# Kernel optimization log

Hardware: AMD Instinct MI355X
Metric: run time of the kernel (lower is better)

## Reference

```python
import jax, jax.numpy as jnp
import numpy as np

N = 50000    # nodes
E = 800000   # edges (avg degree 16)
B = 256      # graphs in the batch (static for segment ops)
H = 128      # feature / hidden width (channels[-2])
NL = 4       # LSTM layers in Set2Set
PS = 4       # Set2Set processing steps
OUT = 2      # channels[-1]


def _bn(h, g, b):
    # BatchNorm1d with batch statistics (training-mode math, biased variance)
    m = h.mean(0)
    v = jnp.mean((h - m) ** 2, 0)
    return (h - m) * jax.lax.rsqrt(v + 1e-5) * g + b


def _gin(x, src, dst, W1, b1, ga1, be1, W2, b2, ga2, be2):
    # GINConv, eps=0: out = MLP(x + sum_{j->i} x_j)
    agg = jax.ops.segment_sum(x[src], dst, num_segments=x.shape[0])
    h = x + agg
    h = jax.nn.relu(_bn(h @ W1.T + b1, ga1, be1))
    h = jax.nn.relu(_bn(h @ W2.T + b2, ga2, be2))
    return h


def _set2set(x, batch, Wih0, Whh0, b0, WihR, WhhR, bR):
    hs = [jnp.zeros((B, H), x.dtype)] * NL
    cs = [jnp.zeros((B, H), x.dtype)] * NL
    q_star = jnp.zeros((B, 2 * H), x.dtype)
    for _ in range(PS):
        inp = q_star
        nhs, ncs = [], []
        for l in range(NL):  # stacked LSTM cells, seq-len 1 per step
            Wih = Wih0 if l == 0 else WihR[l - 1]
            Whh = Whh0 if l == 0 else WhhR[l - 1]
            bb = b0 if l == 0 else bR[l - 1]
            gates = inp @ Wih.T + hs[l] @ Whh.T + bb
            i, f, g, o = jnp.split(gates, 4, axis=-1)  # torch gate order i,f,g,o
            c = jax.nn.sigmoid(f) * cs[l] + jax.nn.sigmoid(i) * jnp.tanh(g)
            h = jax.nn.sigmoid(o) * jnp.tanh(c)
            nhs.append(h); ncs.append(c)
            inp = h
        hs, cs = nhs, ncs
        q = inp  # (B, H) top-layer hidden
        # per-graph segment softmax attention
        e = jnp.sum(x * q[batch], -1)                        # (N,)
        m = jax.ops.segment_max(e, batch, num_segments=B)
        ee = jnp.exp(e - m[batch])
        s = jax.ops.segment_sum(ee, batch, num_segments=B)
        a = ee / s[batch]
        r = jax.ops.segment_sum(a[:, None] * x, batch, num_segments=B)  # (B, H)
        q_star = jnp.concatenate([q, r], -1)
    return q_star


def setup_inputs() -> dict:
    key = jax.random.key(0)
    ks = jax.random.split(key, 16)

    def w(k, shape):
        return jax.random.normal(k, shape, jnp.float32) * 0.05

    d = {}
    d["x"] = jax.random.normal(ks[0], (N, H), jnp.float32)
    d["edge_index"] = jax.random.randint(ks[1], (2, E), 0, N, dtype=jnp.int32)
    d["batch"] = jnp.sort(jax.random.randint(ks[2], (N,), 0, B, dtype=jnp.int32))
    for i, g in enumerate(("g0", "g1")):
        kk = jax.random.split(ks[3 + i], 2)
        d[g + "_W1"] = w(kk[0], (H, H)); d[g + "_b1"] = jnp.zeros((H,), jnp.float32)
        d[g + "_gamma1"] = jnp.ones((H,), jnp.float32); d[g + "_beta1"] = jnp.zeros((H,), jnp.float32)
        d[g + "_W2"] = w(kk[1], (H, H)); d[g + "_b2"] = jnp.zeros((H,), jnp.float32)
        d[g + "_gamma2"] = jnp.ones((H,), jnp.float32); d[g + "_beta2"] = jnp.zeros((H,), jnp.float32)
    d["Wih0"] = w(ks[6], (4 * H, 2 * H))
    d["Whh0"] = w(ks[7], (4 * H, H))
    d["b0"] = jnp.zeros((4 * H,), jnp.float32)
    d["WihR"] = w(ks[8], (NL - 1, 4 * H, H))
    d["WhhR"] = w(ks[9], (NL - 1, 4 * H, H))
    d["bR"] = jnp.zeros((NL - 1, 4 * H), jnp.float32)
    d["lin_W"] = w(ks[10], (OUT, 2 * H))
    d["lin_b"] = jnp.zeros((OUT,), jnp.float32)
    return d


def reference(x, edge_index, batch,
              g0_W1, g0_b1, g0_gamma1, g0_beta1, g0_W2, g0_b2, g0_gamma2, g0_beta2,
              g1_W1, g1_b1, g1_gamma1, g1_beta1, g1_W2, g1_b2, g1_gamma2, g1_beta2,
              Wih0, Whh0, b0, WihR, WhhR, bR, lin_W, lin_b):
    src, dst = edge_index[0], edge_index[1]
    x = _gin(x, src, dst, g0_W1, g0_b1, g0_gamma1, g0_beta1, g0_W2, g0_b2, g0_gamma2, g0_beta2)
    x = _gin(x, src, dst, g1_W1, g1_b1, g1_gamma1, g1_beta1, g1_W2, g1_b2, g1_gamma2, g1_beta2)
    q = _set2set(x, batch, Wih0, Whh0, b0, WihR, WhhR, bR)
    # F.dropout(p=0.1) is identity in eval mode
    return q @ lin_W.T + lin_b
```

## Files before the change

kernel.cpp:

```cpp
#include <hip/hip_runtime.h>
#include <math.h>

#define NN 50000
#define EE 800000
#define BBG 256
#define HHC 128
#define SEG_CAP 448
#define ESC 512
#define NBIN 196
#define NBLK 196

typedef _Float16 half8 __attribute__((ext_vector_type(8)));
typedef _Float16 half4 __attribute__((ext_vector_type(4)));
typedef _Float16 half2v __attribute__((ext_vector_type(2)));

#if defined(__has_builtin)
#if __has_builtin(__builtin_amdgcn_fdot2)
#define USE_FDOT2 1
#endif
#endif

__device__ __forceinline__ float fdot2f(half2v a, half2v b, float c) {
#ifdef USE_FDOT2
  return __builtin_amdgcn_fdot2(a, b, c, false);
#else
  return fmaf((float)a[0], (float)b[0], fmaf((float)a[1], (float)b[1], c));
#endif
}

__device__ __forceinline__ float fsigm(float x) {
  return __builtin_amdgcn_rcpf(1.f + __expf(-x));
}
__device__ __forceinline__ float ftanh(float x) {
  return 1.f - 2.f * __builtin_amdgcn_rcpf(1.f + __expf(2.f * x));
}

__device__ __forceinline__ float4 aff4(float4 v, float4 sc, float4 sh) {
  v.x = fmaxf(fmaf(v.x, sc.x, sh.x), 0.f);
  v.y = fmaxf(fmaf(v.y, sc.y, sh.y), 0.f);
  v.z = fmaxf(fmaf(v.z, sc.z, sh.z), 0.f);
  v.w = fmaxf(fmaf(v.w, sc.w, sh.w), 0.f);
  return v;
}
__device__ __forceinline__ void add4(float4& a, float4 b) {
  a.x += b.x; a.y += b.y; a.z += b.z; a.w += b.w;
}
__device__ __forceinline__ float4 cvt4(half4 h) {
  return make_float4((float)h[0], (float)h[1], (float)h[2], (float)h[3]);
}

__global__ __launch_bounds__(256) void prep_all_kernel(
    const int* __restrict__ batch,
    const int* __restrict__ ei,
    const float* __restrict__ W0, const float* __restrict__ W1,
    const float* __restrict__ W2, const float* __restrict__ W3,
    const float* __restrict__ Wih0, const float* __restrict__ Whh0,
    const float* __restrict__ WihR, const float* __restrict__ WhhR,
    const float* __restrict__ b0, const float* __restrict__ bR,
    const float* __restrict__ xsrc,
    float* __restrict__ stats, int* __restrict__ gptr, int* __restrict__ partial,
    float* __restrict__ ginWT, _Float16* __restrict__ WT0h,
    _Float16* __restrict__ WTRh, float* __restrict__ bc0, float* __restrict__ bcR,
    _Float16* __restrict__ x16a) {
  __shared__ int hist[NBIN];
  int blk = blockIdx.x, tid = threadIdx.x;
  if (blk == 0) {
    ((float4*)stats)[tid] = make_float4(0.f, 0.f, 0.f, 0.f);
    return;
  }
  if (blk <= 196) {
    int i = (blk - 1) * 256 + tid;
    if (i >= NN) return;
    int b = batch[i];
    int prev = (i == 0) ? -1 : batch[i - 1];
    for (int g = prev + 1; g <= b; ++g) gptr[g] = i;
    if (i == NN - 1) {
      for (int g = b + 1; g <= BBG; ++g) gptr[g] = NN;
    }
    return;
  }
  if (blk <= 392) {
    int b = blk - 197;
    if (tid < NBIN) hist[tid] = 0;
    __syncthreads();
    const int4* dst4 = (const int4*)(ei + EE);
#pragma unroll
    for (int c = 0; c < 4; ++c) {
      int idx = b * 1024 + c * 256 + tid;
      if (idx < EE / 4) {
        int4 d = dst4[idx];
        atomicAdd(&hist[d.x >> 8], 1);
        atomicAdd(&hist[d.y >> 8], 1);
        atomicAdd(&hist[d.z >> 8], 1);
        atomicAdd(&hist[d.w >> 8], 1);
      }
    }
    __syncthreads();
    if (tid < NBIN) partial[tid * NBLK + b] = hist[tid];
    return;
  }
  if (blk >= 2961) {
    int i = (blk - 2961) * 256 + tid;
    float4 v = ((const float4*)xsrc)[i];
    half4 h;
    h[0] = (_Float16)v.x; h[1] = (_Float16)v.y;
    h[2] = (_Float16)v.z; h[3] = (_Float16)v.w;
    ((half4*)x16a)[i] = h;
    return;
  }
  int idx = (blk - 393) * 256 + tid;
  if (idx < 65536) {
    int m = idx >> 14;
    int r = idx & 16383;
    int k = r >> 7, o = r & 127;
    const float* W = (m == 0) ? W0 : (m == 1) ? W1 : (m == 2) ? W2 : W3;
    ginWT[idx] = W[o * 128 + k];
  } else if (idx < 262144) {
    int t = idx - 65536;
    int k = t >> 9, op = t & 511;
    int j = op >> 2, g = op & 3;
    int row = g * 128 + j;
    float v = (k < 256) ? Wih0[row * 256 + k] : Whh0[row * 128 + (k - 256)];
    WT0h[((k >> 1) << 10) | (op << 1) | (k & 1)] = (_Float16)v;
  } else if (idx < 655360) {
    int t = idx - 262144;
    int l = t >> 17;
    int rem = t & 131071;
    int k = rem >> 9, op = rem & 511;
    int j = op >> 2, g = op & 3;
    int row = g * 128 + j;
    float v = (k < 128) ? WihR[((size_t)l * 512 + row) * 128 + k]
                        : WhhR[((size_t)l * 512 + row) * 128 + (k - 128)];
    WTRh[((size_t)l << 17) | ((k >> 1) << 10) | (op << 1) | (k & 1)] = (_Float16)v;
  } else {
    int t = idx - 655360;
    if (t < 512) {
      bc0[t] = b0[(t & 3) * 128 + (t >> 2)];
    } else {
      int u = t - 512;
      int l = u >> 9, op = u & 511;
      bcR[u] = bR[l * 512 + (op & 3) * 128 + (op >> 2)];
    }
  }
}


__global__ void scan_partials_kernel(const int* __restrict__ partial,
                                     int* __restrict__ block_base, int* __restrict__ total) {
  __shared__ int buf[256];
  int bin = blockIdx.x, tid = threadIdx.x;
  int v = (tid < NBLK) ? partial[bin * NBLK + tid] : 0;
  buf[tid] = v;
  __syncthreads();
  for (int off = 1; off < 256; off <<= 1) {
    int t = (tid >= off) ? buf[tid - off] : 0;
    __syncthreads();
    buf[tid] += t;
    __syncthreads();
  }
  if (tid < NBLK) block_base[bin * NBLK + tid] = buf[tid] - v;
  if (tid == 255) total[bin] = buf[255];
}

__global__ void scan_totals_kernel(const int* __restrict__ total, int* __restrict__ coarse_base) {
  __shared__ int buf[256];
  int tid = threadIdx.x;
  int v = (tid < NBIN) ? total[tid] : 0;
  buf[tid] = v;
  __syncthreads();
  for (int off = 1; off < 256; off <<= 1) {
    int t = (tid >= off) ? buf[tid - off] : 0;
    __syncthreads();
    buf[tid] += t;
    __syncthreads();
  }
  if (tid < NBIN) coarse_base[tid] = buf[tid] - v;
  if (tid == 255) coarse_base[NBIN] = buf[255];
}

__global__ __launch_bounds__(256) void bucket_scatter_kernel(const int* __restrict__ ei,
                                                             const int* __restrict__ coarse_base,
                                                             const int* __restrict__ block_base,
                                                             int* __restrict__ packed) {
  __shared__ int cursor[NBIN];
  int tid = threadIdx.x, b = blockIdx.x;
  if (tid < NBIN) cursor[tid] = coarse_base[tid] + block_base[tid * NBLK + b];
  __syncthreads();
  const int4* src4 = (const int4*)ei;
  const int4* dst4 = (const int4*)(ei + EE);
#pragma unroll
  for (int c = 0; c < 4; ++c) {
    int idx = b * 1024 + c * 256 + tid;
    if (idx < EE / 4) {
      int4 s = src4[idx];
      int4 d = dst4[idx];
      int p;
      p = atomicAdd(&cursor[d.x >> 8], 1); packed[p] = (s.x << 8) | (d.x & 255);
      p = atomicAdd(&cursor[d.y >> 8], 1); packed[p] = (s.y << 8) | (d.y & 255);
      p = atomicAdd(&cursor[d.z >> 8], 1); packed[p] = (s.z << 8) | (d.z & 255);
      p = atomicAdd(&cursor[d.w >> 8], 1); packed[p] = (s.w << 8) | (d.w & 255);
    }
  }
}

__global__ __launch_bounds__(256) void csr_finalize_kernel(const int* __restrict__ packed,
                                                           const int* __restrict__ coarse_base,
                                                           int* __restrict__ row_start,
                                                           int* __restrict__ csr) {
  __shared__ int fh[256];
  __shared__ int fb[256];
  int bin = blockIdx.x, tid = threadIdx.x;
  int e0 = coarse_base[bin], e1 = coarse_base[bin + 1];
  fh[tid] = 0;
  __syncthreads();
  for (int e = e0 + tid; e < e1; e += 256) atomicAdd(&fh[packed[e] & 255], 1);
  __syncthreads();
  int v = fh[tid];
  fb[tid] = v;
  __syncthreads();
  for (int off = 1; off < 256; off <<= 1) {
    int t = (tid >= off) ? fb[tid - off] : 0;
    __syncthreads();
    fb[tid] += t;
    __syncthreads();
  }
  int excl = fb[tid] - v;
  int node = bin * 256 + tid;
  if (node < NN) row_start[node] = e0 + excl;
  if (bin == NBIN - 1 && tid == 0) row_start[NN] = EE;
  __syncthreads();
  fb[tid] = excl;
  __syncthreads();
  for (int e = e0 + tid; e < e1; e += 256) {
    int p = packed[e];
    int pos = atomicAdd(&fb[p & 255], 1);
    csr[e0 + pos] = p >> 8;
  }
}


template <bool AFF>
__global__ __launch_bounds__(256) void gin_agg_kernel(
    const _Float16* __restrict__ x16, const int* __restrict__ row_start,
    const int* __restrict__ csr,
    const float* __restrict__ stats, const float* __restrict__ gamma,
    const float* __restrict__ beta, float* __restrict__ outp) {
  __shared__ float sc_s[128], sh_s[128];
  if (AFF) {
    int t = threadIdx.x;
    if (t < 128) {
      const float invN = 1.0f / (float)NN;
      float mm = stats[t] * invN;
      float vv = stats[128 + t] * invN - mm * mm;
      float rs = rsqrtf(vv + 1e-5f);
      float sc = gamma[t] * rs;
      sc_s[t] = sc;
      sh_s[t] = beta[t] - mm * sc;
    }
    __syncthreads();
  }
  int node = blockIdx.x * 4 + (threadIdx.x >> 6);
  int lane = threadIdx.x & 63;
  int half = lane >> 5, ln = lane & 31;
  const half4* xh = (const half4*)x16;
  float4 sc4 = make_float4(0.f, 0.f, 0.f, 0.f), sh4 = sc4;
  if (AFF) {
    sc4 = *(const float4*)&sc_s[4 * ln];
    sh4 = *(const float4*)&sh_s[4 * ln];
  }
  int s0 = row_start[node], s1 = row_start[node + 1];
  float4 self = cvt4(xh[(size_t)node * 32 + ln]);
  if (AFF) self = aff4(self, sc4, sh4);
  float4 c0 = make_float4(0.f, 0.f, 0.f, 0.f), c1 = c0, c2 = c0, c3 = c0;
  int cnt = s1 - s0;
  int mainEnd = s0 + (cnt & ~15);
  for (int j = s0; j < mainEnd; j += 16) {
    int i0 = csr[j + half + 0];
    int i1 = csr[j + half + 2];
    int i2 = csr[j + half + 4];
    int i3 = csr[j + half + 6];
    int i4 = csr[j + half + 8];
    int i5 = csr[j + half + 10];
    int i6 = csr[j + half + 12];
    int i7 = csr[j + half + 14];
    half4 h0 = xh[(size_t)i0 * 32 + ln];
    half4 h1 = xh[(size_t)i1 * 32 + ln];
    half4 h2 = xh[(size_t)i2 * 32 + ln];
    half4 h3 = xh[(size_t)i3 * 32 + ln];
    half4 h4 = xh[(size_t)i4 * 32 + ln];
    half4 h5 = xh[(size_t)i5 * 32 + ln];
    half4 h6 = xh[(size_t)i6 * 32 + ln];
    half4 h7 = xh[(size_t)i7 * 32 + ln];
    float4 v0 = cvt4(h0);
    float4 v1 = cvt4(h1);
    float4 v2 = cvt4(h2);
    float4 v3 = cvt4(h3);
    float4 v4 = cvt4(h4);
    float4 v5 = cvt4(h5);
    float4 v6 = cvt4(h6);
    float4 v7 = cvt4(h7);
    if (AFF) {
      v0 = aff4(v0, sc4, sh4); v1 = aff4(v1, sc4, sh4);
      v2 = aff4(v2, sc4, sh4); v3 = aff4(v3, sc4, sh4);
      v4 = aff4(v4, sc4, sh4); v5 = aff4(v5, sc4, sh4);
      v6 = aff4(v6, sc4, sh4); v7 = aff4(v7, sc4, sh4);
    }
    add4(c0, v0); add4(c1, v1); add4(c2, v2); add4(c3, v3);
    add4(c0, v4); add4(c1, v5); add4(c2, v6); add4(c3, v7);
  }
  for (int j = mainEnd + half; j < s1; j += 2) {
    int i = csr[j];
    float4 v = cvt4(xh[(size_t)i * 32 + ln]);
    if (AFF) v = aff4(v, sc4, sh4);
    add4(c0, v);
  }
  float4 t;
  t.x = (c0.x + c1.x) + (c2.x + c3.x);
  t.y = (c0.y + c1.y) + (c2.y + c3.y);
  t.z = (c0.z + c1.z) + (c2.z + c3.z);
  t.w = (c0.w + c1.w) + (c2.w + c3.w);
  t.x += __shfl_xor(t.x, 32);
  t.y += __shfl_xor(t.y, 32);
  t.z += __shfl_xor(t.z, 32);
  t.w += __shfl_xor(t.w, 32);
  t.x += self.x; t.y += self.y; t.z += self.z; t.w += self.w;
  if (half == 0) ((float4*)outp)[(size_t)node * 32 + ln] = t;
}

template <bool BN>
__global__ __launch_bounds__(256) void gemm_gin_kernel(
    const float* __restrict__ A, const float* __restrict__ WT,
    const float* __restrict__ bias,
    const float* __restrict__ stats, const float* __restrict__ gamma,
    const float* __restrict__ beta,
    float* __restrict__ C, _Float16* __restrict__ h16out,
    float* __restrict__ ssum, float* __restrict__ ssq, int M) {
  __shared__ float As[64][132];
  __shared__ float Wt[128][68];
  __shared__ float bsc[128], bsh[128];
  int tid = threadIdx.x;
  if (BN) {
    if (tid < 128) {
      const float invN = 1.0f / (float)NN;
      float mm = stats[tid] * invN;
      float vv = stats[128 + tid] * invN - mm * mm;
      float rs = rsqrtf(vv + 1e-5f);
      float sc = gamma[tid] * rs;
      bsc[tid] = sc;
      bsh[tid] = beta[tid] - mm * sc;
    }
    __syncthreads();
  }
  int tx = tid & 15, ty = tid >> 4;
  int bx = blockIdx.x & 1, by = blockIdx.x >> 1;
  int row0 = by * 64, c0 = bx * 64;
#pragma unroll
  for (int i = 0; i < 8; ++i) {
    int slot = tid + i * 256;
    int r = slot >> 5, k4 = (slot & 31) << 2;
    float4 v = make_float4(0.f, 0.f, 0.f, 0.f);
    if (row0 + r < M) v = *(const float4*)(A + (size_t)(row0 + r) * 128 + k4);
    if (BN) {
      v.x = fmaxf(fmaf(v.x, bsc[k4 + 0], bsh[k4 + 0]), 0.f);
      v.y = fmaxf(fmaf(v.y, bsc[k4 + 1], bsh[k4 + 1]), 0.f);
      v.z = fmaxf(fmaf(v.z, bsc[k4 + 2], bsh[k4 + 2]), 0.f);
      v.w = fmaxf(fmaf(v.w, bsc[k4 + 3], bsh[k4 + 3]), 0.f);
    }
    *(float4*)&As[r][k4] = v;
  }
#pragma unroll
  for (int i = 0; i < 8; ++i) {
    int slot = tid + i * 256;
    int k = slot >> 4, c4 = (slot & 15) << 2;
    *(float4*)&Wt[k][c4] = *(const float4*)(WT + (size_t)k * 128 + c0 + c4);
  }
  __syncthreads();
  float acc[4][4];
#pragma unroll
  for (int i = 0; i < 4; ++i)
#pragma unroll
    for (int j = 0; j < 4; ++j) acc[i][j] = 0.f;
#pragma unroll 4
  for (int kk = 0; kk < 128; kk += 4) {
    float4 w0 = *(const float4*)&Wt[kk + 0][tx << 2];
    float4 w1 = *(const float4*)&Wt[kk + 1][tx << 2];
    float4 w2 = *(const float4*)&Wt[kk + 2][tx << 2];
    float4 w3 = *(const float4*)&Wt[kk + 3][tx << 2];
#pragma unroll
    for (int i = 0; i < 4; ++i) {
      float4 a = *(const float4*)&As[(ty << 2) + i][kk];
      acc[i][0] += a.x * w0.x + a.y * w1.x + a.z * w2.x + a.w * w3.x;
      acc[i][1] += a.x * w0.y + a.y * w1.y + a.z * w2.y + a.w * w3.y;
      acc[i][2] += a.x * w0.z + a.y * w1.z + a.z * w2.z + a.w * w3.z;
      acc[i][3] += a.x * w0.w + a.y * w1.w + a.z * w2.w + a.w * w3.w;
    }
  }
  __syncthreads();
  float b0v = bias[c0 + (tx << 2) + 0];
  float b1v = bias[c0 + (tx << 2) + 1];
  float b2v = bias[c0 + (tx << 2) + 2];
  float b3v = bias[c0 + (tx << 2) + 3];
  float psum[4] = {0.f, 0.f, 0.f, 0.f}, psq[4] = {0.f, 0.f, 0.f, 0.f};
#pragma unroll
  for (int i = 0; i < 4; ++i) {
    int r = row0 + (ty << 2) + i;
    if (r < M) {
      float4 v;
      v.x = acc[i][0] + b0v; v.y = acc[i][1] + b1v;
      v.z = acc[i][2] + b2v; v.w = acc[i][3] + b3v;
      if (C) *(float4*)(C + (size_t)r * 128 + c0 + (tx << 2)) = v;
      if (h16out) {
        half4 hv;
        hv[0] = (_Float16)v.x; hv[1] = (_Float16)v.y;
        hv[2] = (_Float16)v.z; hv[3] = (_Float16)v.w;
        *(half4*)(h16out + (size_t)r * 128 + c0 + (tx << 2)) = hv;
      }
      psum[0] += v.x; psum[1] += v.y; psum[2] += v.z; psum[3] += v.w;
      psq[0] += v.x * v.x; psq[1] += v.y * v.y; psq[2] += v.z * v.z; psq[3] += v.w * v.w;
    }
  }
  float* red = &As[0][0];
#pragma unroll
  for (int j = 0; j < 4; ++j) {
    red[ty * 68 + (tx << 2) + j] = psum[j];
    red[1088 + ty * 68 + (tx << 2) + j] = psq[j];
  }
  __syncthreads();
  if (tid < 64) {
    float s = 0.f, sq = 0.f;
#pragma unroll
    for (int t = 0; t < 16; ++t) { s += red[t * 68 + tid]; sq += red[1088 + t * 68 + tid]; }
    atomicAdd(&ssum[c0 + tid], s);
    atomicAdd(&ssq[c0 + tid], sq);
  }
}

__global__ void __launch_bounds__(1024) set2set_kernel(
    const float* __restrict__ x, const int* __restrict__ gptr,
    const float* __restrict__ stats, const float* __restrict__ gamma,
    const float* __restrict__ beta,
    const _Float16* __restrict__ WT0h, const _Float16* __restrict__ WTRh,
    const float* __restrict__ bc0, const float* __restrict__ bcR,
    float* __restrict__ ebuf,
    const float* __restrict__ linW, const float* __restrict__ linb,
    float* __restrict__ out) {
  __shared__ half2v xs[SEG_CAP * 64];
  __shared__ float wpart[16][512];
  __shared__ float gates[512];
  __shared__ half2v inp2[192];
  __shared__ float hcs[4][128];
  __shared__ float ccs[4][128];
  __shared__ float qst[256];
  __shared__ float es[ESC];
  __shared__ float bsc[128], bsh[128];
  __shared__ float wred[16];
  __shared__ float smax_s, ssum_s;
  __shared__ float fred[2][4];

  int g = blockIdx.x, tid = threadIdx.x;
  int w16 = tid >> 6, lane = tid & 63;

  if (tid < 128) {
    const float invN = 1.0f / (float)NN;
    float mm = stats[tid] * invN;
    float vv = stats[128 + tid] * invN - mm * mm;
    float rs = rsqrtf(vv + 1e-5f);
    float sc = gamma[tid] * rs;
    bsc[tid] = sc;
    bsh[tid] = beta[tid] - mm * sc;
#pragma unroll
    for (int l = 0; l < 4; ++l) { hcs[l][tid] = 0.f; ccs[l][tid] = 0.f; }
  }
  if (tid < 256) qst[tid] = 0.f;
  __syncthreads();

  int s0 = gptr[g], s1 = gptr[g + 1];
  int seg = s1 - s0;
  int ncache = seg < SEG_CAP ? seg : SEG_CAP;
  const float2* x2 = (const float2*)x;
  float sc0 = bsc[2 * lane], sc1 = bsc[2 * lane + 1];
  float sh0 = bsh[2 * lane], sh1 = bsh[2 * lane + 1];
  for (int n = w16; n < ncache; n += 16) {
    float2 v = x2[(size_t)(s0 + n) * 64 + lane];
    half2v h;
    h[0] = (_Float16)fmaxf(fmaf(v.x, sc0, sh0), 0.f);
    h[1] = (_Float16)fmaxf(fmaf(v.y, sc1, sh1), 0.f);
    xs[n * 64 + lane] = h;
  }
  __syncthreads();

  int s_ = tid >> 6, cg = tid & 63;

  for (int step = 0; step < 4; ++step) {
    for (int cell = 0; cell < 4; ++cell) {
      const _Float16* WTh; const float* bias; int KP2;
      if (cell == 0) {
        WTh = WT0h; bias = bc0; KP2 = 12;
        if (tid < 192) {
          int k = tid << 1;
          float va, vb;
          if (k < 256) { va = qst[k]; vb = qst[k + 1]; }
          else { va = hcs[0][k - 256]; vb = hcs[0][k - 255]; }
          half2v h; h[0] = (_Float16)va; h[1] = (_Float16)vb;
          inp2[tid] = h;
        }
      } else {
        WTh = WTRh + (size_t)(cell - 1) * 131072;
        bias = bcR + (cell - 1) * 512; KP2 = 8;
        if (tid < 128) {
          int k = tid << 1;
          float va, vb;
          if (k < 128) { va = hcs[cell - 1][k]; vb = hcs[cell - 1][k + 1]; }
          else { va = hcs[cell][k - 128]; vb = hcs[cell][k - 127]; }
          half2v h; h[0] = (_Float16)va; h[1] = (_Float16)vb;
          inp2[tid] = h;
        }
      }
      __syncthreads();
      if (step == 0 && cell == 0) {
        if (tid < 512) gates[tid] = bias[tid];
        __syncthreads();
      } else {
        int se = (s_ + g) & 15;
        int k20 = se * KP2;
        float a0 = 0.f, a1 = 0.f, a2 = 0.f, a3 = 0.f;
        float a4 = 0.f, a5 = 0.f, a6 = 0.f, a7 = 0.f;
        if (step != 0 || se < 8) {
          const char* wb = (const char*)WTh + (size_t)k20 * 2048 + (cg << 5);
#pragma unroll 4
          for (int k2 = 0; k2 < KP2; ++k2) {
            uint4 wa = *(const uint4*)(wb + (size_t)k2 * 2048);
            uint4 wc = *(const uint4*)(wb + (size_t)k2 * 2048 + 16);
            half2v i2 = inp2[k20 + k2];
            a0 = fdot2f(i2, __builtin_bit_cast(half2v, wa.x), a0);
            a1 = fdot2f(i2, __builtin_bit_cast(half2v, wa.y), a1);
            a2 = fdot2f(i2, __builtin_bit_cast(half2v, wa.z), a2);
            a3 = fdot2f(i2, __builtin_bit_cast(half2v, wa.w), a3);
            a4 = fdot2f(i2, __builtin_bit_cast(half2v, wc.x), a4);
            a5 = fdot2f(i2, __builtin_bit_cast(half2v, wc.y), a5);
            a6 = fdot2f(i2, __builtin_bit_cast(half2v, wc.z), a6);
            a7 = fdot2f(i2, __builtin_bit_cast(half2v, wc.w), a7);
          }
        }
        *(float4*)&wpart[s_][cg << 3] = make_float4(a0, a1, a2, a3);
        *(float4*)(&wpart[s_][cg << 3] + 4) = make_float4(a4, a5, a6, a7);
        __syncthreads();
        if (tid < 512) {
          float acc = bias[tid];
#pragma unroll
          for (int s = 0; s < 16; ++s) acc += wpart[s][tid];
          gates[tid] = acc;
        }
        __syncthreads();
      }
      if (tid < 128) {
        int j = tid;
        float gi = gates[4 * j + 0];
        float gf = gates[4 * j + 1];
        float gc = gates[4 * j + 2];
        float go = gates[4 * j + 3];
        float cp = ccs[cell][j];
        float si = fsigm(gi);
        float sf = fsigm(gf);
        float so = fsigm(go);
        float cn = sf * cp + si * ftanh(gc);
        ccs[cell][j] = cn;
        hcs[cell][j] = so * ftanh(cn);
      }
      __syncthreads();
    }
    float* rpart = &wpart[0][0];
    float qx = hcs[3][2 * lane], qy = hcs[3][2 * lane + 1];
    half2v q2; q2[0] = (_Float16)qx; q2[1] = (_Float16)qy;
    float wmax = -3.0e38f;
    for (int n = w16; n < seg; n += 16) {
      float e;
      if (n < ncache) {
        e = fdot2f(xs[n * 64 + lane], q2, 0.f);
      } else {
        float2 v = x2[(size_t)(s0 + n) * 64 + lane];
        float vx = fmaxf(fmaf(v.x, sc0, sh0), 0.f);
        float vy = fmaxf(fmaf(v.y, sc1, sh1), 0.f);
        e = vx * qx + vy * qy;
      }
#pragma unroll
      for (int sh = 32; sh; sh >>= 1) e += __shfl_xor(e, sh);
      if (lane == 0) { if (n < ESC) es[n] = e; else ebuf[s0 + n] = e; }
      wmax = fmaxf(wmax, e);
    }
    if (lane == 0) wred[w16] = wmax;
    __syncthreads();
    if (tid == 0) {
      float m = wred[0];
#pragma unroll
      for (int t = 1; t < 16; ++t) m = fmaxf(m, wred[t]);
      smax_s = m;
    }
    __syncthreads();
    float m = smax_s;
    float loc = 0.f;
    for (int n = tid; n < seg; n += 1024) {
      float e = (n < ESC) ? es[n] : ebuf[s0 + n];
      float ex = __expf(e - m);
      if (n < ESC) es[n] = ex; else ebuf[s0 + n] = ex;
      loc += ex;
    }
#pragma unroll
    for (int sh = 32; sh; sh >>= 1) loc += __shfl_xor(loc, sh);
    __syncthreads();
    if (lane == 0) wred[w16] = loc;
    __syncthreads();
    if (tid == 0) {
      float s = 0.f;
#pragma unroll
      for (int t = 0; t < 16; ++t) s += wred[t];
      ssum_s = s;
    }
    __syncthreads();
    float inv = 1.0f / ssum_s;
    float rx = 0.f, ry = 0.f;
    for (int n = w16; n < seg; n += 16) {
      float ex = (n < ESC) ? es[n] : ebuf[s0 + n];
      float coef = ex * inv;
      float vx, vy;
      if (n < ncache) {
        half2v v2 = xs[n * 64 + lane];
        vx = (float)v2[0]; vy = (float)v2[1];
      } else {
        float2 v = x2[(size_t)(s0 + n) * 64 + lane];
        vx = fmaxf(fmaf(v.x, sc0, sh0), 0.f);
        vy = fmaxf(fmaf(v.y, sc1, sh1), 0.f);
      }
      rx += coef * vx; ry += coef * vy;
    }
    rpart[w16 * 128 + 2 * lane] = rx;
    rpart[w16 * 128 + 2 * lane + 1] = ry;
    __syncthreads();
    if (tid < 128) {
      float r = 0.f;
#pragma unroll
      for (int t = 0; t < 16; ++t) r += rpart[t * 128 + tid];
      qst[tid] = hcs[3][tid];
      qst[128 + tid] = r;
    }
    __syncthreads();
  }
  if (tid < 256) {
    float val = qst[tid];
    float p0 = val * linW[tid];
    float p1 = val * linW[256 + tid];
#pragma unroll
    for (int sh = 32; sh; sh >>= 1) { p0 += __shfl_xor(p0, sh); p1 += __shfl_xor(p1, sh); }
    if (lane == 0) { fred[0][w16] = p0; fred[1][w16] = p1; }
  }
  __syncthreads();
  if (tid == 0) {
    out[2 * g + 0] = fred[0][0] + fred[0][1] + fred[0][2] + fred[0][3] + linb[0];
    out[2 * g + 1] = fred[1][0] + fred[1][1] + fred[1][2] + fred[1][3] + linb[1];
  }
}


extern "C" void kernel_launch(void* const* d_in, const int* in_sizes, int n_in,
                              void* d_out, int out_size, void* d_ws, size_t ws_size,
                              hipStream_t stream) {
  const float* x = (const float*)d_in[0];
  const int* ei = (const int*)d_in[1];
  const int* batch = (const int*)d_in[2];
  const float* gW[4]  = {(const float*)d_in[3],  (const float*)d_in[7],
                         (const float*)d_in[11], (const float*)d_in[15]};
  const float* gb[4]  = {(const float*)d_in[4],  (const float*)d_in[8],
                         (const float*)d_in[12], (const float*)d_in[16]};
  const float* gga[4] = {(const float*)d_in[5],  (const float*)d_in[9],
                         (const float*)d_in[13], (const float*)d_in[17]};
  const float* gbe[4] = {(const float*)d_in[6],  (const float*)d_in[10],
                         (const float*)d_in[14], (const float*)d_in[18]};
  const float* Wih0 = (const float*)d_in[19];
  const float* Whh0 = (const float*)d_in[20];
  const float* b0   = (const float*)d_in[21];
  const float* WihR = (const float*)d_in[22];
  const float* WhhR = (const float*)d_in[23];
  const float* bR   = (const float*)d_in[24];
  const float* linW = (const float*)d_in[25];
  const float* linb = (const float*)d_in[26];
  float* out = (float*)d_out;

  char* base = (char*)d_ws;
  size_t off = 0;
  auto allocf = [&](size_t n) { float* p = (float*)(base + off); off += n * sizeof(float); return p; };
  float* xa    = allocf(6400000);
  float* xb    = allocf(6400000);
  float* ginWT = allocf(65536);
  _Float16* WT0h = (_Float16*)(base + off); off += 196608 * 2;
  _Float16* WTRh = (_Float16*)(base + off); off += 393216 * 2;
  _Float16* x16a = (_Float16*)(base + off); off += 6400000 * 2;
  _Float16* x16b = (_Float16*)(base + off); off += 6400000 * 2;
  float* bc0   = allocf(512);
  float* bcR   = allocf(1536);
  float* ebuf  = allocf(50000);
  float* stats = allocf(1024);
  int* row_start = (int*)(base + off); off += 50004 * 4;
  int* gptr = (int*)(base + off); off += 260 * 4;
  int* csr = (int*)(base + off); off += 800000 * 4;
  int* packed = (int*)(base + off); off += 800000 * 4;
  int* partial = (int*)(base + off); off += NBIN * NBLK * 4;
  int* block_base = (int*)(base + off); off += NBIN * NBLK * 4;
  int* total = (int*)(base + off); off += 256 * 4;
  int* coarse_base = (int*)(base + off); off += 260 * 4;
  (void)ws_size; (void)in_sizes; (void)n_in; (void)out_size;

  prep_all_kernel<<<9211, 256, 0, stream>>>(batch, ei, gW[0], gW[1], gW[2], gW[3],
                                            Wih0, Whh0, WihR, WhhR, b0, bR, x,
                                            stats, gptr, partial, ginWT, WT0h, WTRh,
                                            bc0, bcR, x16a);
  scan_partials_kernel<<<NBIN, 256, 0, stream>>>(partial, block_base, total);
  scan_totals_kernel<<<1, 256, 0, stream>>>(total, coarse_base);
  bucket_scatter_kernel<<<NBLK, 256, 0, stream>>>(ei, coarse_base, block_base, packed);
  csr_finalize_kernel<<<NBIN, 256, 0, stream>>>(packed, coarse_base, row_start, csr);

  gin_agg_kernel<false><<<12500, 256, 0, stream>>>(x16a, row_start, csr,
                                                   nullptr, nullptr, nullptr, xb);
  gemm_gin_kernel<false><<<1564, 256, 0, stream>>>(xb, ginWT + 0 * 16384, gb[0],
                                                   nullptr, nullptr, nullptr,
                                                   xa, nullptr, stats + 0, stats + 128, NN);
  gemm_gin_kernel<true><<<1564, 256, 0, stream>>>(xa, ginWT + 1 * 16384, gb[1],
                                                  stats + 0, gga[0], gbe[0],
                                                  nullptr, x16b, stats + 256, stats + 384, NN);
  gin_agg_kernel<true><<<12500, 256, 0, stream>>>(x16b, row_start, csr,
                                                  stats + 256, gga[1], gbe[1], xa);
  gemm_gin_kernel<false><<<1564, 256, 0, stream>>>(xa, ginWT + 2 * 16384, gb[2],
                                                   nullptr, nullptr, nullptr,
                                                   xb, nullptr, stats + 512, stats + 640, NN);
  gemm_gin_kernel<true><<<1564, 256, 0, stream>>>(xb, ginWT + 3 * 16384, gb[3],
                                                  stats + 512, gga[2], gbe[2],
                                                  xa, nullptr, stats + 768, stats + 896, NN);

  set2set_kernel<<<256, 1024, 0, stream>>>(xa, gptr, stats + 768, gga[3], gbe[3],
                                           WT0h, WTRh, bc0, bcR, ebuf, linW, linb, out);
}
```

Measured before the change: 495.6 us.

## Replace FP32 SIMT GIN GEMMs with fp16 MFMA kernels and fp16 intermediates

The four GIN linear layers now run on MFMA 16x16x32 f16 instructions. Weights are stored untransposed in fp16 and held in registers, and each block handles four 16-row tiles. The intermediate activation between the two linears of each GIN layer is written as fp16 (x16a) instead of fp32, which reduces memory traffic. BN statistics are reduced with wave shuffles. This trades accuracy, since inputs are rounded to fp16, and the output stores are strided scalar writes rather than vectorized ones.

```diff
diff --git a/kernel.cpp b/kernel.cpp
--- a/kernel.cpp
+++ b/kernel.cpp
@@ -13,6 +13,7 @@
 typedef _Float16 half8 __attribute__((ext_vector_type(8)));
 typedef _Float16 half4 __attribute__((ext_vector_type(4)));
 typedef _Float16 half2v __attribute__((ext_vector_type(2)));
+typedef float f32x4 __attribute__((ext_vector_type(4)));
 
 #if defined(__has_builtin)
 #if __has_builtin(__builtin_amdgcn_fdot2)
@@ -59,7 +60,7 @@
     const float* __restrict__ b0, const float* __restrict__ bR,
     const float* __restrict__ xsrc,
     float* __restrict__ stats, int* __restrict__ gptr, int* __restrict__ partial,
-    float* __restrict__ ginWT, _Float16* __restrict__ WT0h,
+    _Float16* __restrict__ ginWh, _Float16* __restrict__ WT0h,
     _Float16* __restrict__ WTRh, float* __restrict__ bc0, float* __restrict__ bcR,
     _Float16* __restrict__ x16a) {
   __shared__ int hist[NBIN];
@@ -112,9 +113,8 @@
   if (idx < 65536) {
     int m = idx >> 14;
     int r = idx & 16383;
-    int k = r >> 7, o = r & 127;
     const float* W = (m == 0) ? W0 : (m == 1) ? W1 : (m == 2) ? W2 : W3;
-    ginWT[idx] = W[o * 128 + k];
+    ginWh[idx] = (_Float16)W[r];
   } else if (idx < 262144) {
     int t = idx - 65536;
     int k = t >> 9, op = t & 511;
@@ -327,17 +327,16 @@
   if (half == 0) ((float4*)outp)[(size_t)node * 32 + ln] = t;
 }
 
-template <bool BN>
-__global__ __launch_bounds__(256) void gemm_gin_kernel(
-    const float* __restrict__ A, const float* __restrict__ WT,
+template <bool BN, bool AH>
+__global__ __launch_bounds__(256) void gemm_gin_mfma_kernel(
+    const float* __restrict__ A, const _Float16* __restrict__ A16,
+    const _Float16* __restrict__ Wh,
     const float* __restrict__ bias,
     const float* __restrict__ stats, const float* __restrict__ gamma,
     const float* __restrict__ beta,
     float* __restrict__ C, _Float16* __restrict__ h16out,
-    float* __restrict__ ssum, float* __restrict__ ssq, int M) {
-  __shared__ float As[64][132];
-  __shared__ float Wt[128][68];
-  __shared__ float bsc[128], bsh[128];
+    float* __restrict__ ssum, float* __restrict__ ssq) {
+  __shared__ float bsc_s[128], bsh_s[128];
   int tid = threadIdx.x;
   if (BN) {
     if (tid < 128) {
@@ -346,92 +345,104 @@
       float vv = stats[128 + tid] * invN - mm * mm;
       float rs = rsqrtf(vv + 1e-5f);
       float sc = gamma[tid] * rs;
-      bsc[tid] = sc;
-      bsh[tid] = beta[tid] - mm * sc;
-    }
-    __syncthreads();
-  }
-  int tx = tid & 15, ty = tid >> 4;
-  int bx = blockIdx.x & 1, by = blockIdx.x >> 1;
-  int row0 = by * 64, c0 = bx * 64;
-#pragma unroll
-  for (int i = 0; i < 8; ++i) {
-    int slot = tid + i * 256;
-    int r = slot >> 5, k4 = (slot & 31) << 2;
-    float4 v = make_float4(0.f, 0.f, 0.f, 0.f);
-    if (row0 + r < M) v = *(const float4*)(A + (size_t)(row0 + r) * 128 + k4);
-    if (BN) {
-      v.x = fmaxf(fmaf(v.x, bsc[k4 + 0], bsh[k4 + 0]), 0.f);
-      v.y = fmaxf(fmaf(v.y, bsc[k4 + 1], bsh[k4 + 1]), 0.f);
-      v.z = fmaxf(fmaf(v.z, bsc[k4 + 2], bsh[k4 + 2]), 0.f);
-      v.w = fmaxf(fmaf(v.w, bsc[k4 + 3], bsh[k4 + 3]), 0.f);
-    }
-    *(float4*)&As[r][k4] = v;
-  }
-#pragma unroll
-  for (int i = 0; i < 8; ++i) {
-    int slot = tid + i * 256;
-    int k = slot >> 4, c4 = (slot & 15) << 2;
-    *(float4*)&Wt[k][c4] = *(const float4*)(WT + (size_t)k * 128 + c0 + c4);
-  }
-  __syncthreads();
-  float acc[4][4];
-#pragma unroll
-  for (int i = 0; i < 4; ++i)
-#pragma unroll
-    for (int j = 0; j < 4; ++j) acc[i][j] = 0.f;
-#pragma unroll 4
-  for (int kk = 0; kk < 128; kk += 4) {
-    float4 w0 = *(const float4*)&Wt[kk + 0][tx << 2];
-    float4 w1 = *(const float4*)&Wt[kk + 1][tx << 2];
-    float4 w2 = *(const float4*)&Wt[kk + 2][tx << 2];
-    float4 w3 = *(const float4*)&Wt[kk + 3][tx << 2];
+      bsc_s[tid] = sc;
+      bsh_s[tid] = beta[tid] - mm * sc;
+    }
+    __syncthreads();
+  }
+  int w = tid >> 6, l = tid & 63;
+  int lr = l & 15, lg = l >> 4;
+  int cb = w * 32;
+  half8 bf0[4], bf1[4];
+#pragma unroll
+  for (int ks = 0; ks < 4; ++ks) {
+    int k = ks * 32 + lg * 8;
+    bf0[ks] = *(const half8*)(Wh + (size_t)(cb + lr) * 128 + k);
+    bf1[ks] = *(const half8*)(Wh + (size_t)(cb + 16 + lr) * 128 + k);
+  }
+  float bv0 = bias[cb + lr], bv1 = bias[cb + 16 + lr];
+  float ps0 = 0.f, pq0 = 0.f, ps1 = 0.f, pq1 = 0.f;
+  int t0 = blockIdx.x * 4;
+  for (int t = 0; t < 4; ++t) {
+    int tile = t0 + t;
+    if (tile >= 3125) break;
+    int r = tile * 16 + lr;
+    half8 af[4];
+#pragma unroll
+    for (int ks = 0; ks < 4; ++ks) {
+      int k0 = ks * 32 + lg * 8;
+      if constexpr (AH) {
+        half8 ah = *(const half8*)(A16 + (size_t)r * 128 + k0);
+        if constexpr (BN) {
+          float4 s0 = *(const float4*)&bsc_s[k0];
+          float4 s1 = *(const float4*)&bsc_s[k0 + 4];
+          float4 h0 = *(const float4*)&bsh_s[k0];
+          float4 h1 = *(const float4*)&bsh_s[k0 + 4];
+          half8 o;
+          o[0] = (_Float16)fmaxf(fmaf((float)ah[0], s0.x, h0.x), 0.f);
+          o[1] = (_Float16)fmaxf(fmaf((float)ah[1], s0.y, h0.y), 0.f);
+          o[2] = (_Float16)fmaxf(fmaf((float)ah[2], s0.z, h0.z), 0.f);
+          o[3] = (_Float16)fmaxf(fmaf((float)ah[3], s0.w, h0.w), 0.f);
+          o[4] = (_Float16)fmaxf(fmaf((float)ah[4], s1.x, h1.x), 0.f);
+          o[5] = (_Float16)fmaxf(fmaf((float)ah[5], s1.y, h1.y), 0.f);
+          o[6] = (_Float16)fmaxf(fmaf((float)ah[6], s1.z, h1.z), 0.f);
+          o[7] = (_Float16)fmaxf(fmaf((float)ah[7], s1.w, h1.w), 0.f);
+          af[ks] = o;
+        } else {
+          af[ks] = ah;
+        }
+      } else {
+        float4 a0 = *(const float4*)(A + (size_t)r * 128 + k0);
+        float4 a1 = *(const float4*)(A + (size_t)r * 128 + k0 + 4);
+        if constexpr (BN) {
+          float4 s0 = *(const float4*)&bsc_s[k0];
+          float4 s1 = *(const float4*)&bsc_s[k0 + 4];
+          float4 h0 = *(const float4*)&bsh_s[k0];
+          float4 h1 = *(const float4*)&bsh_s[k0 + 4];
+          a0 = aff4(a0, s0, h0);
+          a1 = aff4(a1, s1, h1);
+        }
+        half8 o;
+        o[0] = (_Float16)a0.x; o[1] = (_Float16)a0.y;
+        o[2] = (_Float16)a0.z; o[3] = (_Float16)a0.w;
+        o[4] = (_Float16)a1.x; o[5] = (_Float16)a1.y;
+        o[6] = (_Float16)a1.z; o[7] = (_Float16)a1.w;
+        af[ks] = o;
+      }
+    }
+    f32x4 acc0 = {0.f, 0.f, 0.f, 0.f};
+    f32x4 acc1 = {0.f, 0.f, 0.f, 0.f};
+#pragma unroll
+    for (int ks = 0; ks < 4; ++ks) {
+      acc0 = __builtin_amdgcn_mfma_f32_16x16x32_f16(af[ks], bf0[ks], acc0, 0, 0, 0);
+      acc1 = __builtin_amdgcn_mfma_f32_16x16x32_f16(af[ks], bf1[ks], acc1, 0, 0, 0);
+    }
 #pragma unroll
     for (int i = 0; i < 4; ++i) {
-      float4 a = *(const float4*)&As[(ty << 2) + i][kk];
-      acc[i][0] += a.x * w0.x + a.y * w1.x + a.z * w2.x + a.w * w3.x;
-      acc[i][1] += a.x * w0.y + a.y * w1.y + a.z * w2.y + a.w * w3.y;
-      acc[i][2] += a.x * w0.z + a.y * w1.z + a.z * w2.z + a.w * w3.z;
-      acc[i][3] += a.x * w0.w + a.y * w1.w + a.z * w2.w + a.w * w3.w;
-    }
-  }
-  __syncthreads();
-  float b0v = bias[c0 + (tx << 2) + 0];
-  float b1v = bias[c0 + (tx << 2) + 1];
-  float b2v = bias[c0 + (tx << 2) + 2];
-  float b3v = bias[c0 + (tx << 2) + 3];
-  float psum[4] = {0.f, 0.f, 0.f, 0.f}, psq[4] = {0.f, 0.f, 0.f, 0.f};
-#pragma unroll
-  for (int i = 0; i < 4; ++i) {
-    int r = row0 + (ty << 2) + i;
-    if (r < M) {
-      float4 v;
-      v.x = acc[i][0] + b0v; v.y = acc[i][1] + b1v;
-      v.z = acc[i][2] + b2v; v.w = acc[i][3] + b3v;
-      if (C) *(float4*)(C + (size_t)r * 128 + c0 + (tx << 2)) = v;
+      int rr = tile * 16 + lg * 4 + i;
+      float v0 = acc0[i] + bv0;
+      float v1 = acc1[i] + bv1;
+      if (C) {
+        C[(size_t)rr * 128 + cb + lr] = v0;
+        C[(size_t)rr * 128 + cb + 16 + lr] = v1;
+      }
       if (h16out) {
-        half4 hv;
-        hv[0] = (_Float16)v.x; hv[1] = (_Float16)v.y;
-        hv[2] = (_Float16)v.z; hv[3] = (_Float16)v.w;
-        *(half4*)(h16out + (size_t)r * 128 + c0 + (tx << 2)) = hv;
-      }
-      psum[0] += v.x; psum[1] += v.y; psum[2] += v.z; psum[3] += v.w;
-      psq[0] += v.x * v.x; psq[1] += v.y * v.y; psq[2] += v.z * v.z; psq[3] += v.w * v.w;
-    }
-  }
-  float* red = &As[0][0];
-#pragma unroll
-  for (int j = 0; j < 4; ++j) {
-    red[ty * 68 + (tx << 2) + j] = psum[j];
-    red[1088 + ty * 68 + (tx << 2) + j] = psq[j];
-  }
-  __syncthreads();
-  if (tid < 64) {
-    float s = 0.f, sq = 0.f;
-#pragma unroll
-    for (int t = 0; t < 16; ++t) { s += red[t * 68 + tid]; sq += red[1088 + t * 68 + tid]; }
-    atomicAdd(&ssum[c0 + tid], s);
-    atomicAdd(&ssq[c0 + tid], sq);
+        h16out[(size_t)rr * 128 + cb + lr] = (_Float16)v0;
+        h16out[(size_t)rr * 128 + cb + 16 + lr] = (_Float16)v1;
+      }
+      ps0 += v0; pq0 += v0 * v0;
+      ps1 += v1; pq1 += v1 * v1;
+    }
+  }
+  ps0 += __shfl_xor(ps0, 16); ps0 += __shfl_xor(ps0, 32);
+  pq0 += __shfl_xor(pq0, 16); pq0 += __shfl_xor(pq0, 32);
+  ps1 += __shfl_xor(ps1, 16); ps1 += __shfl_xor(ps1, 32);
+  pq1 += __shfl_xor(pq1, 16); pq1 += __shfl_xor(pq1, 32);
+  if (lg == 0) {
+    atomicAdd(&ssum[cb + lr], ps0);
+    atomicAdd(&ssq[cb + lr], pq0);
+    atomicAdd(&ssum[cb + 16 + lr], ps1);
+    atomicAdd(&ssq[cb + 16 + lr], pq1);
   }
 }
 
@@ -690,7 +701,7 @@
   auto allocf = [&](size_t n) { float* p = (float*)(base + off); off += n * sizeof(float); return p; };
   float* xa    = allocf(6400000);
   float* xb    = allocf(6400000);
-  float* ginWT = allocf(65536);
+  _Float16* ginWh = (_Float16*)(base + off); off += 65536 * 2;
   _Float16* WT0h = (_Float16*)(base + off); off += 196608 * 2;
   _Float16* WTRh = (_Float16*)(base + off); off += 393216 * 2;
   _Float16* x16a = (_Float16*)(base + off); off += 6400000 * 2;
@@ -711,7 +722,7 @@
 
   prep_all_kernel<<<9211, 256, 0, stream>>>(batch, ei, gW[0], gW[1], gW[2], gW[3],
                                             Wih0, Whh0, WihR, WhhR, b0, bR, x,
-                                            stats, gptr, partial, ginWT, WT0h, WTRh,
+                                            stats, gptr, partial, ginWh, WT0h, WTRh,
                                             bc0, bcR, x16a);
   scan_partials_kernel<<<NBIN, 256, 0, stream>>>(partial, block_base, total);
   scan_totals_kernel<<<1, 256, 0, stream>>>(total, coarse_base);
@@ -720,20 +731,24 @@
 
   gin_agg_kernel<false><<<12500, 256, 0, stream>>>(x16a, row_start, csr,
                                                    nullptr, nullptr, nullptr, xb);
-  gemm_gin_kernel<false><<<1564, 256, 0, stream>>>(xb, ginWT + 0 * 16384, gb[0],
-                                                   nullptr, nullptr, nullptr,
-                                                   xa, nullptr, stats + 0, stats + 128, NN);
-  gemm_gin_kernel<true><<<1564, 256, 0, stream>>>(xa, ginWT + 1 * 16384, gb[1],
-                                                  stats + 0, gga[0], gbe[0],
-                                                  nullptr, x16b, stats + 256, stats + 384, NN);
+  gemm_gin_mfma_kernel<false, false><<<782, 256, 0, stream>>>(
+      xb, nullptr, ginWh + 0 * 16384, gb[0],
+      nullptr, nullptr, nullptr,
+      nullptr, x16a, stats + 0, stats + 128);
+  gemm_gin_mfma_kernel<true, true><<<782, 256, 0, stream>>>(
+      nullptr, x16a, ginWh + 1 * 16384, gb[1],
+      stats + 0, gga[0], gbe[0],
+      nullptr, x16b, stats + 256, stats + 384);
   gin_agg_kernel<true><<<12500, 256, 0, stream>>>(x16b, row_start, csr,
                                                   stats + 256, gga[1], gbe[1], xa);
-  gemm_gin_kernel<false><<<1564, 256, 0, stream>>>(xa, ginWT + 2 * 16384, gb[2],
-                                                   nullptr, nullptr, nullptr,
-                                                   xb, nullptr, stats + 512, stats + 640, NN);
-  gemm_gin_kernel<true><<<1564, 256, 0, stream>>>(xb, ginWT + 3 * 16384, gb[3],
-                                                  stats + 512, gga[2], gbe[2],
-                                                  xa, nullptr, stats + 768, stats + 896, NN);
+  gemm_gin_mfma_kernel<false, false><<<782, 256, 0, stream>>>(
+      xa, nullptr, ginWh + 2 * 16384, gb[2],
+      nullptr, nullptr, nullptr,
+      nullptr, x16a, stats + 512, stats + 640);
+  gemm_gin_mfma_kernel<true, true><<<782, 256, 0, stream>>>(
+      nullptr, x16a, ginWh + 3 * 16384, gb[3],
+      stats + 512, gga[2], gbe[2],
+      xa, nullptr, stats + 768, stats + 896);
 
   set2set_kernel<<<256, 1024, 0, stream>>>(xa, gptr, stats + 768, gga[3], gbe[3],
                                            WT0h, WTRh, bc0, bcR, ebuf, linW, linb, out);
```

Measured after the change: 442.9 us. -10.6%, faster.
